# Performance work log

Measured on AMD Instinct MI355X. Metric: run time of the kernel, lower is better.

Reference implementation:

```python
import jax, jax.numpy as jnp
import numpy as np

COORD_W, WIDTH_W, VALID_W = 5.0, 1.0, 1.0  # module init defaults
COST_COORD_W, COST_WIDTH_W = 5.0, 1.0      # hardcoded in compute_cost_matrix


def _hungarian(cost):
    """Pure-numpy linear_sum_assignment (Jonker-Volgenant style, e-maxx variant).
    cost: [R, C] float. Returns (row_ind, col_ind) matching scipy semantics
    (min(R, C) pairs minimizing total cost)."""
    cost = np.asarray(cost, dtype=np.float64)
    transposed = cost.shape[0] > cost.shape[1]
    C = cost.T if transposed else cost
    n, m = C.shape  # n <= m
    u = np.zeros(n + 1)
    v = np.zeros(m + 1)
    p = np.zeros(m + 1, dtype=np.int64)   # p[j] = 1-indexed row assigned to col j
    way = np.zeros(m + 1, dtype=np.int64)
    for i in range(1, n + 1):
        p[0] = i
        j0 = 0
        minv = np.full(m + 1, np.inf)
        used = np.zeros(m + 1, dtype=bool)
        while True:
            used[j0] = True
            i0 = p[j0]
            jf = np.nonzero(~used[1:])[0] + 1  # free columns (1-indexed)
            cur = C[i0 - 1, jf - 1] - u[i0] - v[jf]
            upd = cur < minv[jf]
            minv[jf] = np.where(upd, cur, minv[jf])
            way[jf[upd]] = j0
            j1 = jf[np.argmin(minv[jf])]
            delta = minv[j1]
            u[p[used]] += delta
            v[used] -= delta
            minv[jf] -= delta
            j0 = j1
            if p[j0] == 0:
                break
        while j0:
            j1 = way[j0]
            p[j0] = p[j1]
            j0 = j1
    col4row = np.zeros(n, dtype=np.int64)
    for j in range(1, m + 1):
        if p[j] > 0:
            col4row[p[j] - 1] = j - 1
    rows = np.arange(n, dtype=np.int64)
    return (col4row, rows) if transposed else (rows, col4row)


def _compute_matching(pred_strokes, targets):
    """Per-batch Hungarian matching on the (detached) cost matrix.
    Returns padded pred idx P [B,S], gt idx G [B,S], match mask M [B,S], num_gt N [B]."""
    ps = np.asarray(pred_strokes)
    tg = np.asarray(targets)
    B, S, _ = ps.shape
    P = np.zeros((B, S), dtype=np.int64)
    G = np.zeros((B, S), dtype=np.int64)
    M = np.zeros((B, S), dtype=np.float32)
    N = np.zeros((B,), dtype=np.float32)
    for b in range(B):
        valid = np.nonzero(tg[b, :, 10] > 0.5)[0]
        ng = len(valid)
        N[b] = ng
        if ng == 0:
            continue
        gt = tg[b, valid, :10]                      # [ng, 10]
        d = np.abs(ps[b, :, None, :] - gt[None])    # [S, ng, 10]
        cost = COST_COORD_W * d[..., :8].sum(-1) + COST_WIDTH_W * d[..., 8:10].sum(-1)
        pi, gi = _hungarian(cost)
        P[b, :ng] = pi
        G[b, :ng] = valid[gi]
        M[b, :ng] = 1.0
    return P, G, M, N


def _loss(pred_strokes, pred_validity, targets, P, G, M, N):
    gt_strokes = targets[..., :10]
    gt_val = targets[..., 10:11]
    mp = jnp.take_along_axis(pred_strokes, P[..., None], axis=1)  # [B,S,10]
    mg = jnp.take_along_axis(gt_strokes, G[..., None], axis=1)    # [B,S,10]
    ad = jnp.abs(mp - mg) * M[..., None]
    ng = jnp.maximum(N, 1.0)
    coord = ad[..., :8].sum(axis=(1, 2)) / (ng * 8.0)             # per-batch L1 mean
    width = ad[..., 8:10].sum(axis=(1, 2)) / (ng * 2.0)
    # BCE with torch-style log clamp at -100
    logp = jnp.clip(jnp.log(pred_validity), -100.0)
    log1p = jnp.clip(jnp.log(1.0 - pred_validity), -100.0)
    bce = (-(gt_val * logp + (1.0 - gt_val) * log1p)).mean(axis=(1, 2))
    loss_b = jnp.where(N > 0, COORD_W * coord + WIDTH_W * width + VALID_W * bce, bce)
    return loss_b.mean()


def setup_inputs() -> dict:
    key = jax.random.key(0)
    k1, k2, k3 = jax.random.split(key, 3)
    B, S = 256, 64
    return {
        "pred_strokes": jax.random.uniform(k1, (B, S, 10), dtype=jnp.float32),
        "pred_validity": jax.random.uniform(k2, (B, S, 1), dtype=jnp.float32),
        "targets": jax.random.uniform(k3, (B, S, 11), dtype=jnp.float32),
    }


def reference(pred_strokes, pred_validity, targets):
    P, G, M, N = _compute_matching(pred_strokes, targets)
    return _loss(pred_strokes, pred_validity, targets,
                 jnp.asarray(P), jnp.asarray(G), jnp.asarray(M), jnp.asarray(N))
```

## Files before the change

kernel.cpp:

```cpp
#include <hip/hip_runtime.h>
#include <math.h>


#define SS 64
#define LDS_FENCE() asm volatile("s_waitcnt lgkmcnt(0)" ::: "memory")

__device__ __forceinline__ int rlane_i(int x, int lane) {
    return __builtin_amdgcn_readlane(x, lane);
}
__device__ __forceinline__ double rlane_d(double x, int lane) {
    return __hiloint2double(rlane_i(__double2hiint(x), lane),
                            rlane_i(__double2loint(x), lane));
}

template<int CTRL>
__device__ __forceinline__ unsigned mstep(unsigned x) {
    const unsigned y = (unsigned)__builtin_amdgcn_update_dpp(
        (int)x, (int)x, CTRL, 0xF, 0xF, false);
    return x < y ? x : y;
}
__device__ __forceinline__ unsigned wave_min_u32_to63(unsigned x) {
    x = mstep<0x111>(x);
    x = mstep<0x112>(x);
    x = mstep<0x114>(x);
    x = mstep<0x118>(x);
    x = mstep<0x142>(x);
    x = mstep<0x143>(x);
    return x;
}

__global__ __launch_bounds__(64) void detr_match_loss_kernel(
    const float* __restrict__ pred_strokes,
    const float* __restrict__ pred_validity,
    const float* __restrict__ targets,
    double* __restrict__ loss_ws,
    unsigned* __restrict__ counter,
    float* __restrict__ out, int B)
{
    const int b = blockIdx.x;
    const int t = threadIdx.x;
    const float* ps = pred_strokes  + (size_t)b * SS * 10;
    const float* pv = pred_validity + (size_t)b * SS;
    const float* tg = targets      + (size_t)b * SS * 11;

    __shared__ double Cs[SS * SS];
    __shared__ int    col4row[SS];

    float tgv[11];
#pragma unroll
    for (int k = 0; k < 11; ++k) tgv[k] = tg[t * 11 + k];
    const float gv    = tgv[10];
    const bool  valid = gv > 0.5f;
    const unsigned long long vmask = __ballot(valid);
    const int ng = __popcll(vmask);

    double bterm;
    {
        const float pvv = pv[t];
        const float lp  = fmaxf(logf(pvv), -100.0f);
        const float l1p = fmaxf(logf(1.0f - pvv), -100.0f);
        bterm = -((double)gv * (double)lp + (double)(1.0f - gv) * (double)l1p);
    }

    double csum = 0.0, wsum = 0.0;

    if (ng > 0) {
        float pr[10];
#pragma unroll
        for (int k = 0; k < 10; ++k) pr[k] = ps[t * 10 + k];

        double u_reg = 0.0;
        int    p_j   = 0;
        unsigned long long colclaim = 0ull;
        unsigned long long freerows = 0ull;
        unsigned long long vm = vmask;

        for (int i = 0; i < ng; ++i) {
            const int vrow = __ffsll(vm) - 1;
            vm &= vm - 1;
            float g[10];
#pragma unroll
            for (int k = 0; k < 10; ++k)
                g[k] = __uint_as_float(
                    (unsigned)rlane_i(__float_as_int(tgv[k]), vrow));
            float d[10];
#pragma unroll
            for (int k = 0; k < 10; ++k) d[k] = fabsf(pr[k] - g[k]);
            const float cs = ((d[0] + d[1]) + (d[2] + d[3]))
                           + ((d[4] + d[5]) + (d[6] + d[7]));
            const float wd = d[8] + d[9];
            float c;
            {
#pragma clang fp contract(off)
                c = 5.0f * cs + wd;
            }
            Cs[i * SS + t] = (double)c;

            const unsigned key = __float_as_uint(c);
            const unsigned mst = (unsigned)rlane_i(
                (int)wave_min_u32_to63(key), 63);
            const unsigned long long rbal = __ballot(key == mst);
            const int jstar = __ffsll(rbal) - 1;
            if (t == i) u_reg = (double)__uint_as_float(mst);
            if (!((colclaim >> jstar) & 1ull)) {
                colclaim |= 1ull << jstar;
                if (t == jstar) p_j = i + 1;
            } else {
                freerows |= 1ull << i;
            }
        }

        double v_j = 0.0;
        int nr0 = freerows ? (__ffsll(freerows) - 1) : -1;
        double Chead = (nr0 >= 0) ? Cs[nr0 * SS + t] : 0.0;

        while (freerows) {
            const int r0 = nr0;
            freerows &= freerows - 1;
            nr0 = freerows ? (__ffsll(freerows) - 1) : -1;
            const int i = r0 + 1;

            double minv_j   = __builtin_inf();
            int    way_j    = 0;
            bool   used_j   = false;
            bool   row_used = (t == r0);
            double u0       = rlane_d(u_reg, r0);
            int    j0       = 0;
            double Cval     = Chead;

            const double Chead_next = (nr0 >= 0) ? Cs[nr0 * SS + t] : 0.0;

            for (;;) {
                used_j = used_j || (t + 1 == j0);
                const double cur = (Cval - u0) - v_j;
                if (!used_j && cur < minv_j) { minv_j = cur; way_j = j0; }

                const int      hi  = __double2hiint(minv_j);
                const int      s31 = hi >> 31;
                unsigned key = (unsigned)(hi ^ (s31 | (int)0x80000000));
                if (used_j) key = 0xFFFFFFFFu;
                const unsigned hstar = (unsigned)rlane_i(
                    (int)wave_min_u32_to63(key), 63);
                unsigned long long bal = __ballot(key == hstar);
                int j1 = __ffsll(bal);
                int i1 = rlane_i(p_j, j1 - 1);

                double C_next = 0.0;
                if (i1 != 0) C_next = Cs[(i1 - 1) * SS + t];

                if (__popcll(bal) > 1) {
                    const unsigned lraw = (unsigned)__double2loint(minv_j);
                    const unsigned lo   = (key == hstar)
                                        ? (s31 ? ~lraw : lraw) : 0xFFFFFFFFu;
                    const unsigned lstar = (unsigned)rlane_i(
                        (int)wave_min_u32_to63(lo), 63);
                    bal = __ballot(key == hstar && lo == lstar);
                    j1  = __ffsll(bal);
                    i1  = rlane_i(p_j, j1 - 1);
                    if (i1 != 0) C_next = Cs[(i1 - 1) * SS + t];
                }

                const int hmin = (hstar & 0x80000000u)
                               ? (int)(hstar & 0x7FFFFFFFu) : (int)~hstar;
                const int lmin = rlane_i(__double2loint(minv_j), j1 - 1);
                const double delta  = __hiloint2double(hmin, lmin);
                const double u_next = (i1 != 0) ? rlane_d(u_reg, i1 - 1) : 0.0;

                if (row_used) u_reg += delta;
                if (used_j)   v_j   -= delta;
                else          minv_j -= delta;
                row_used = row_used || (t == i1 - 1);

                j0 = j1;
                if (i1 == 0) break;
                u0 = u_next; Cval = C_next;
            }

            int jj = j0;
            while (jj != 0) {
                const int jp   = rlane_i(way_j, jj - 1);
                const int pnew = (jp == 0) ? i : rlane_i(p_j, jp - 1);
                if (t == jj - 1) p_j = pnew;
                jj = jp;
            }
            Chead = Chead_next;
        }

        if (p_j > 0) col4row[p_j - 1] = t;
        LDS_FENCE();

        if (valid) {
            const int r = __popcll(vmask & ((1ull << t) - 1ull));
            const float* mp = ps + col4row[r] * 10;
#pragma unroll
            for (int k = 0; k < 8; ++k) csum += (double)fabsf(mp[k] - tgv[k]);
            wsum = (double)fabsf(mp[8] - tgv[8]) + (double)fabsf(mp[9] - tgv[9]);
        }
    }

    double s0 = csum, s1 = wsum, s2 = bterm;
#pragma unroll
    for (int off = 1; off < 64; off <<= 1) {
        s0 += __shfl_xor(s0, off, 64);
        s1 += __shfl_xor(s1, off, 64);
        s2 += __shfl_xor(s2, off, 64);
    }

    unsigned prev = 0;
    if (t == 0) {
        const double bce = s2 / 64.0;
        const double loss = (ng > 0)
            ? 5.0 * (s0 / ((double)ng * 8.0)) + (s1 / ((double)ng * 2.0)) + bce
            : bce;
        __hip_atomic_store(&loss_ws[b], loss,
                           __ATOMIC_RELEASE, __HIP_MEMORY_SCOPE_AGENT);
        prev = __hip_atomic_fetch_add(counter, 1u,
                                      __ATOMIC_ACQ_REL, __HIP_MEMORY_SCOPE_AGENT);
    }
    prev = (unsigned)rlane_i((int)prev, 0);

    if (prev == (unsigned)(B - 1)) {
        double x = 0.0;
        for (int idx = t; idx < B; idx += SS)
            x += __hip_atomic_load(&loss_ws[idx],
                                   __ATOMIC_RELAXED, __HIP_MEMORY_SCOPE_AGENT);
#pragma unroll
        for (int off = 1; off < 64; off <<= 1) x += __shfl_xor(x, off, 64);
        if (t == 0) out[0] = (float)(x / (double)B);
    }
}

extern "C" void kernel_launch(void* const* d_in, const int* in_sizes, int n_in,
                              void* d_out, int out_size, void* d_ws, size_t ws_size,
                              hipStream_t stream) {
    const float* ps = (const float*)d_in[0];
    const float* pv = (const float*)d_in[1];
    const float* tg = (const float*)d_in[2];
    float* out = (float*)d_out;
    const int B = in_sizes[0] / (SS * 10);

    double*   ws  = (double*)d_ws;
    unsigned* cnt = (unsigned*)((char*)d_ws + (size_t)B * sizeof(double));
    hipMemsetAsync(cnt, 0, sizeof(unsigned), stream);

    detr_match_loss_kernel<<<B, SS, 0, stream>>>(ps, pv, tg, ws, cnt, out, B);
}
```

Measured before the change: 87.11 us.

## Add auction-style augmenting row reduction before shortest-path Hungarian phase

```diff
diff --git a/kernel.cpp b/kernel.cpp
--- a/kernel.cpp
+++ b/kernel.cpp
@@ -27,6 +27,32 @@
     x = mstep<0x142>(x);
     x = mstep<0x143>(x);
     return x;
+}
+
+struct MinRes { double val; int lane; };
+__device__ __forceinline__ MinRes wave_argmin_f64(double x, bool excl) {
+    const int hi  = __double2hiint(x);
+    const int s31 = hi >> 31;
+    unsigned key  = (unsigned)(hi ^ (s31 | (int)0x80000000));
+    if (excl) key = 0xFFFFFFFFu;
+    const unsigned hstar = (unsigned)rlane_i((int)wave_min_u32_to63(key), 63);
+    unsigned long long bal = __ballot(key == hstar);
+    int jl = __ffsll(bal) - 1;
+    const int hmin = (hstar & 0x80000000u) ? (int)(hstar & 0x7FFFFFFFu)
+                                           : (int)~hstar;
+    int lmin;
+    if (__popcll(bal) > 1) {
+        const unsigned lraw = (unsigned)__double2loint(x);
+        const unsigned lo   = (key == hstar) ? (s31 ? ~lraw : lraw)
+                                             : 0xFFFFFFFFu;
+        const unsigned lstar = (unsigned)rlane_i((int)wave_min_u32_to63(lo), 63);
+        bal  = __ballot(key == hstar && lo == lstar);
+        jl   = __ffsll(bal) - 1;
+        lmin = (hmin < 0) ? (int)~lstar : (int)lstar;
+    } else {
+        lmin = rlane_i(__double2loint(x), jl);
+    }
+    MinRes r; r.val = __hiloint2double(hmin, lmin); r.lane = jl; return r;
 }
 
 __global__ __launch_bounds__(64) void detr_match_loss_kernel(
@@ -70,6 +96,7 @@
         for (int k = 0; k < 10; ++k) pr[k] = ps[t * 10 + k];
 
         double u_reg = 0.0;
+        double v_j   = 0.0;
         int    p_j   = 0;
         unsigned long long colclaim = 0ull;
         unsigned long long freerows = 0ull;
@@ -110,7 +137,32 @@
             }
         }
 
-        double v_j = 0.0;
+        {
+            unsigned long long arr = freerows;
+            int steps = 0;
+            const int cap = 2 * __popcll(arr) + 4;
+            int    pre  = -1;
+            double Cpre = 0.0;
+            while (arr && steps < cap) {
+                const int r0 = __ffsll(arr) - 1;
+                arr &= arr - 1; ++steps;
+                const double Crow = (r0 == pre) ? Cpre : Cs[r0 * SS + t];
+                pre  = arr ? (__ffsll(arr) - 1) : -1;
+                Cpre = (pre >= 0) ? Cs[pre * SS + t] : 0.0;
+
+                const double r = Crow - v_j;
+                const MinRes m1 = wave_argmin_f64(r, false);
+                const MinRes m2 = wave_argmin_f64(r, t == m1.lane);
+                if (t == r0) u_reg = m2.val;
+                if (m1.val < m2.val && t == m1.lane)
+                    v_j -= (m2.val - m1.val);
+                const int k = rlane_i(p_j, m1.lane);
+                if (t == m1.lane) p_j = r0 + 1;
+                if (k) arr |= 1ull << (k - 1);
+            }
+            freerows = arr;
+        }
+
         int nr0 = freerows ? (__ffsll(freerows) - 1) : -1;
         double Chead = (nr0 >= 0) ? Cs[nr0 * SS + t] : 0.0;
 
@@ -135,35 +187,14 @@
                 const double cur = (Cval - u0) - v_j;
                 if (!used_j && cur < minv_j) { minv_j = cur; way_j = j0; }
 
-                const int      hi  = __double2hiint(minv_j);
-                const int      s31 = hi >> 31;
-                unsigned key = (unsigned)(hi ^ (s31 | (int)0x80000000));
-                if (used_j) key = 0xFFFFFFFFu;
-                const unsigned hstar = (unsigned)rlane_i(
-                    (int)wave_min_u32_to63(key), 63);
-                unsigned long long bal = __ballot(key == hstar);
-                int j1 = __ffsll(bal);
-                int i1 = rlane_i(p_j, j1 - 1);
+                const MinRes m = wave_argmin_f64(minv_j, used_j);
+                const int j1 = m.lane + 1;
+                const int i1 = rlane_i(p_j, m.lane);
 
                 double C_next = 0.0;
                 if (i1 != 0) C_next = Cs[(i1 - 1) * SS + t];
 
-                if (__popcll(bal) > 1) {
-                    const unsigned lraw = (unsigned)__double2loint(minv_j);
-                    const unsigned lo   = (key == hstar)
-                                        ? (s31 ? ~lraw : lraw) : 0xFFFFFFFFu;
-                    const unsigned lstar = (unsigned)rlane_i(
-                        (int)wave_min_u32_to63(lo), 63);
-                    bal = __ballot(key == hstar && lo == lstar);
-                    j1  = __ffsll(bal);
-                    i1  = rlane_i(p_j, j1 - 1);
-                    if (i1 != 0) C_next = Cs[(i1 - 1) * SS + t];
-                }
-
-                const int hmin = (hstar & 0x80000000u)
-                               ? (int)(hstar & 0x7FFFFFFFu) : (int)~hstar;
-                const int lmin = rlane_i(__double2loint(minv_j), j1 - 1);
-                const double delta  = __hiloint2double(hmin, lmin);
+                const double delta  = m.val;
                 const double u_next = (i1 != 0) ? rlane_d(u_reg, i1 - 1) : 0.0;
 
                 if (row_used) u_reg += delta;
```

New measurement: 91.24 us. 4.8% more time.
